# Optimization experiments

Hardware: AMD Instinct MI355X
Metric: run time of the kernel (lower is better)

The kernel has to match this reference:

```python
import jax, jax.numpy as jnp
import numpy as np

ML, KS, L = 3, 7, 7  # mL, kernelSize, L = 2*mL+1


def _conv(img, kern, pad, groups=1):
    # img: [N,C,H,W], kern: [O, C//groups, kh, kw]
    return jax.lax.conv_general_dilated(
        img, kern, (1, 1), [(pad, pad), (pad, pad)],
        dimension_numbers=("NCHW", "OIHW", "NCHW"),
        feature_group_count=groups)


def setup_inputs() -> dict:
    key = jax.random.key(0)
    ks = jax.random.split(key, 16)
    B, MU = 64, 256
    lin = lambda k, fi, fo: (jax.random.normal(k, (fi, fo), jnp.float32) / np.sqrt(fi)).astype(jnp.float32)
    return {
        "x": jax.random.normal(ks[0], (B, 1, MU, MU), jnp.float32),
        "f": jax.random.normal(ks[1], (B, 1, MU, MU), jnp.float32),
        "kernelA": jax.random.normal(ks[2], (B, 1, 3, 3), jnp.float32),
        "fc1_w1": lin(ks[3], 9, 200), "fc1_b1": jnp.zeros((200,), jnp.float32),
        "fc1_w2": lin(ks[4], 200, ML * KS * KS), "fc1_b2": jnp.zeros((ML * KS * KS,), jnp.float32),
        "fc2_w1": lin(ks[5], 9, 200), "fc2_b1": jnp.zeros((200,), jnp.float32),
        "fc2_w2": lin(ks[6], 200, ML * ML * KS * KS), "fc2_b2": jnp.zeros((ML * ML * KS * KS,), jnp.float32),
    }


def reference(x, f, kernelA, fc1_w1, fc1_b1, fc1_w2, fc1_b2, fc2_w1, fc2_b1, fc2_w2, fc2_b2):
    B, _, mu, _ = x.shape
    pad = KS // 2

    # residual r = f - A x   (per-sample 3x3 stencil conv, grouped)
    r = f - jax.vmap(lambda xi, ki: _conv(xi[None], ki[None], 1)[0])(x, kernelA)  # [B,1,mu,mu]

    # meta-MLPs produce per-sample dynamic conv kernels from the 3x3 stencil
    kA = kernelA.reshape(B, 9)
    h1 = jax.nn.relu(kA @ fc1_w1 + fc1_b1)
    w1 = (h1 @ fc1_w2 + fc1_b2).reshape(B, ML, 1, KS, KS)
    h2 = jax.nn.relu(kA @ fc2_w1 + fc2_b1)
    w2 = (h2 @ fc2_w2 + fc2_b2).reshape(B, ML, ML, KS, KS)

    # per-sample dynamic convs (batched via vmap)
    G1 = jax.vmap(lambda ri, wi: _conv(ri[None], wi, pad)[0])(r, w1)    # [B,mL,mu,mu]
    G2 = jax.vmap(lambda gi, wi: _conv(gi[None], wi, pad)[0])(G1, w2)   # [B,mL,mu,mu]
    G = jnp.concatenate([r, G1, G2], axis=1)                            # [B,L,mu,mu]

    # S = A G : apply per-sample stencil to each of the L channels (depthwise)
    S = jax.vmap(lambda gi, ki: _conv(gi[None], jnp.broadcast_to(ki[None], (L, 1, 3, 3)), 1, groups=L)[0])(G, kernelA)
    S = S.reshape(B, L, mu * mu)
    Gf = G.reshape(B, L, mu * mu)
    lr = r.reshape(B, mu * mu, 1)

    # normal equations: (S S^T) K = S r, tiny [L,L] solve per sample
    M = jnp.einsum("bln,bmn->blm", S, S)    # [B,L,L]
    b = jnp.matmul(S, lr)                   # [B,L,1]
    K = jnp.linalg.solve(M, b)              # [B,L,1]

    x_new = x + jnp.matmul(K.transpose(0, 2, 1), Gf).reshape(B, 1, mu, mu)
    return x_new
```

## Files before the change

kernel.cpp:

```cpp
#include <hip/hip_runtime.h>

#define MU 256
#define NPIX (MU*MU)
#define ML 3
#define KS 7
#define LCH 7
#define NENT 35
#define RBLK 64

__global__ void mlp_kernel(const float* __restrict__ kernelA,
                           const float* __restrict__ fc1_w1, const float* __restrict__ fc1_b1,
                           const float* __restrict__ fc1_w2, const float* __restrict__ fc1_b2,
                           const float* __restrict__ fc2_w1, const float* __restrict__ fc2_b1,
                           const float* __restrict__ fc2_w2, const float* __restrict__ fc2_b2,
                           float* __restrict__ w1_out, float* __restrict__ w2_out) {
    int b = blockIdx.x;
    int t = threadIdx.x;
    __shared__ float kA[9];
    __shared__ float h1[200], h2[200];
    if (t < 9) kA[t] = kernelA[b*9 + t];
    __syncthreads();
    if (t < 200) {
        float s1 = fc1_b1[t], s2 = fc2_b1[t];
        #pragma unroll
        for (int i = 0; i < 9; ++i) {
            s1 += kA[i] * fc1_w1[i*200 + t];
            s2 += kA[i] * fc2_w1[i*200 + t];
        }
        h1[t] = fmaxf(s1, 0.f);
        h2[t] = fmaxf(s2, 0.f);
    }
    __syncthreads();
    if (t < 147) {
        float s = fc1_b2[t];
        for (int i = 0; i < 200; ++i) s += h1[i] * fc1_w2[i*147 + t];
        w1_out[b*147 + t] = s;
    }
    for (int o = t; o < 441; o += 256) {
        float s = fc2_b2[o];
        for (int i = 0; i < 200; ++i) s += h2[i] * fc2_w2[i*441 + o];
        w2_out[b*441 + o] = s;
    }
}

__global__ __launch_bounds__(256, 4) void residual_kernel(
        const float* __restrict__ x, const float* __restrict__ f,
        const float* __restrict__ kA, float* __restrict__ r) {
    int b = blockIdx.z;
    __shared__ float tile[18][72];
    int tx = threadIdx.x, ty = threadIdx.y;
    int tid = ty*64 + tx;
    float k[9];
    #pragma unroll
    for (int i = 0; i < 9; ++i) k[i] = kA[b*9 + i];
    int x0 = blockIdx.x*64, ysub = blockIdx.y*16;
    const float* xb = x + (size_t)b*NPIX;

    for (int u = tid; u < 18*18; u += 256) {
        int row = u / 18, q4 = u % 18;
        int yy = ysub + row - 1;
        int xx = x0 - 4 + q4*4;
        float4 vv = make_float4(0.f, 0.f, 0.f, 0.f);
        if (yy >= 0 && yy < MU && xx >= 0 && xx < MU)
            vv = *(const float4*)(xb + yy*MU + xx);
        *(float4*)&tile[row][q4*4] = vv;
    }
    __syncthreads();

    int ry = ty*4;
    float S0 = 0.f, S1 = 0.f, S2 = 0.f, S3 = 0.f;
    #pragma unroll
    for (int t = 0; t < 6; ++t) {
        float v0 = tile[ry + t][tx + 3];
        float v1 = tile[ry + t][tx + 4];
        float v2 = tile[ry + t][tx + 5];
        float e0 = v0*k[0] + v1*k[1] + v2*k[2];
        float e1 = v0*k[3] + v1*k[4] + v2*k[5];
        float e2 = v0*k[6] + v1*k[7] + v2*k[8];
        if (t == 0) { S0 += e0; }
        if (t == 1) { S1 += e0; S0 += e1; }
        if (t == 2) { S2 += e0; S1 += e1; S0 += e2; }
        if (t == 3) { S3 += e0; S2 += e1; S1 += e2; }
        if (t == 4) {           S3 += e1; S2 += e2; }
        if (t == 5) {                     S3 += e2; }
    }
    float Sv[4] = {S0, S1, S2, S3};
    #pragma unroll
    for (int dy = 0; dy < 4; ++dy) {
        size_t p = (size_t)b*NPIX + (size_t)(ysub + ry + dy)*MU + x0 + tx;
        r[p] = f[p] - Sv[dy];
    }
}

__global__ __launch_bounds__(256) void conv7_g1(
        const float* __restrict__ r, const float* __restrict__ w1,
        float* __restrict__ G1) {
    int b = blockIdx.z;
    __shared__ float tile[22][136];
    int tx = threadIdx.x;
    int ty = threadIdx.y;
    int tid = ty*64 + tx;
    int x0 = blockIdx.x*128, y0 = blockIdx.y*16;
    const float* rb = r + (size_t)b*NPIX;
    const float* wgt = w1 + (size_t)b*147;

    for (int u = tid; u < 22*34; u += 256) {
        int row = u / 34, q4 = u % 34;
        int yy = y0 + row - 3;
        int xx = x0 - 4 + q4*4;
        float4 vv = make_float4(0.f, 0.f, 0.f, 0.f);
        if (yy >= 0 && yy < MU && xx >= 0 && xx < MU)
            vv = *(const float4*)(rb + yy*MU + xx);
        *(float4*)&tile[row][q4*4] = vv;
    }
    __syncthreads();

    float accA[3][4], accB[3][4];
    #pragma unroll
    for (int co = 0; co < 3; ++co)
        #pragma unroll
        for (int dy = 0; dy < 4; ++dy) { accA[co][dy] = 0.f; accB[co][dy] = 0.f; }

    int ry = ty*4;
    #pragma unroll
    for (int ir = 0; ir < 10; ++ir) {
        float v[10];
        #pragma unroll
        for (int h = 0; h < 5; ++h)
            *(float2*)&v[h*2] = *(float2*)&tile[ry + ir][2*tx + h*2];
        #pragma unroll
        for (int dy = 0; dy < 4; ++dy) {
            int i = ir - dy;
            if (i >= 0 && i <= 6) {
                #pragma unroll
                for (int co = 0; co < 3; ++co)
                    #pragma unroll
                    for (int j = 0; j < 7; ++j) {
                        float w = wgt[(co*7 + i)*7 + j];
                        accA[co][dy] += v[1 + j] * w;
                        accB[co][dy] += v[2 + j] * w;
                    }
            }
        }
    }
    #pragma unroll
    for (int dy = 0; dy < 4; ++dy) {
        size_t p = (size_t)b*3*NPIX + (size_t)(y0 + ry + dy)*MU + x0 + 2*tx;
        #pragma unroll
        for (int co = 0; co < 3; ++co)
            *(float2*)&G1[p + (size_t)co*NPIX] = make_float2(accA[co][dy], accB[co][dy]);
    }
}

__global__ __launch_bounds__(256) void conv7_g2(
        const float* __restrict__ G1, const float* __restrict__ w2,
        float* __restrict__ G2) {
    int b = blockIdx.z;
    __shared__ float tile[3][10][136];
    int tx = threadIdx.x;
    int ty = threadIdx.y;
    int tid = ty*64 + tx;
    int x0 = blockIdx.x*128, y0 = blockIdx.y*4;
    const float* g1b = G1 + (size_t)b*3*NPIX;
    const float* wgt = w2 + (size_t)b*441;

    for (int u = tid; u < 3*10*34; u += 256) {
        int c = u / (10*34);
        int rem = u % (10*34);
        int row = rem / 34, q4 = rem % 34;
        int yy = y0 + row - 3;
        int xx = x0 - 4 + q4*4;
        float4 vv = make_float4(0.f, 0.f, 0.f, 0.f);
        if (yy >= 0 && yy < MU && xx >= 0 && xx < MU)
            vv = *(const float4*)(g1b + (size_t)c*NPIX + yy*MU + xx);
        *(float4*)&tile[c][row][q4*4] = vv;
    }
    __syncthreads();

    float accA[3], accB[3];
    #pragma unroll
    for (int co = 0; co < 3; ++co) { accA[co] = 0.f; accB[co] = 0.f; }

    #pragma unroll
    for (int c = 0; c < 3; ++c) {
        #pragma unroll
        for (int ir = 0; ir < 7; ++ir) {
            float v[10];
            #pragma unroll
            for (int h = 0; h < 5; ++h)
                *(float2*)&v[h*2] = *(float2*)&tile[c][ty + ir][2*tx + h*2];
            #pragma unroll
            for (int co = 0; co < 3; ++co)
                #pragma unroll
                for (int j = 0; j < 7; ++j) {
                    float w = wgt[((co*3 + c)*7 + ir)*7 + j];
                    accA[co] += v[1 + j] * w;
                    accB[co] += v[2 + j] * w;
                }
        }
    }
    size_t p = (size_t)b*3*NPIX + (size_t)(y0 + ty)*MU + x0 + 2*tx;
    #pragma unroll
    for (int co = 0; co < 3; ++co)
        *(float2*)&G2[p + (size_t)co*NPIX] = make_float2(accA[co], accB[co]);
}

__global__ __launch_bounds__(256, 4) void reduce_kernel(
        const float* __restrict__ r, const float* __restrict__ G1,
        const float* __restrict__ G2, const float* __restrict__ kA,
        float* __restrict__ partial) {
    int b = blockIdx.z;
    __shared__ float tile[7][18][72];
    __shared__ float wsum[NENT][4];
    int tx = threadIdx.x;
    int ty = threadIdx.y;
    int tid = ty*64 + tx;
    float k[9];
    #pragma unroll
    for (int i = 0; i < 9; ++i) k[i] = kA[b*9 + i];

    const float* srcs[7] = {
        r  + (size_t)b*NPIX,
        G1 + (size_t)b*3*NPIX, G1 + (size_t)b*3*NPIX + NPIX, G1 + (size_t)b*3*NPIX + 2*NPIX,
        G2 + (size_t)b*3*NPIX, G2 + (size_t)b*3*NPIX + NPIX, G2 + (size_t)b*3*NPIX + 2*NPIX
    };

    int x0 = blockIdx.x*64;
    int ysub = blockIdx.y*16;

    #pragma unroll
    for (int c = 0; c < 7; ++c) {
        const float* src = srcs[c];
        for (int u = tid; u < 18*18; u += 256) {
            int row = u / 18, q4 = u % 18;
            int yy = ysub + row - 1;
            int xx = x0 - 4 + q4*4;
            float4 vv = make_float4(0.f, 0.f, 0.f, 0.f);
            if (yy >= 0 && yy < MU && xx >= 0 && xx < MU)
                vv = *(const float4*)(src + yy*MU + xx);
            *(float4*)&tile[c][row][q4*4] = vv;
        }
    }
    __syncthreads();

    float acc[64];
    #pragma unroll
    for (int e = 0; e < 64; ++e) acc[e] = 0.f;

    int ry = ty*4;
    float S_all[7][4];
    #pragma unroll
    for (int c = 0; c < 7; ++c) {
        float S0 = 0.f, S1 = 0.f, S2 = 0.f, S3 = 0.f;
        #pragma unroll
        for (int t = 0; t < 6; ++t) {
            float v0 = tile[c][ry + t][tx + 3];
            float v1 = tile[c][ry + t][tx + 4];
            float v2 = tile[c][ry + t][tx + 5];
            float e0 = v0*k[0] + v1*k[1] + v2*k[2];
            float e1 = v0*k[3] + v1*k[4] + v2*k[5];
            float e2 = v0*k[6] + v1*k[7] + v2*k[8];
            if (t == 0) { S0 += e0; }
            if (t == 1) { S1 += e0; S0 += e1; }
            if (t == 2) { S2 += e0; S1 += e1; S0 += e2; }
            if (t == 3) { S3 += e0; S2 += e1; S1 += e2; }
            if (t == 4) {           S3 += e1; S2 += e2; }
            if (t == 5) {                     S3 += e2; }
        }
        S_all[c][0] = S0; S_all[c][1] = S1; S_all[c][2] = S2; S_all[c][3] = S3;
    }
    #pragma unroll
    for (int dy = 0; dy < 4; ++dy) {
        float rv = tile[0][ry + dy + 1][tx + 4];
        int idx = 0;
        #pragma unroll
        for (int l = 0; l < 7; ++l) {
            #pragma unroll
            for (int m = l; m < 7; ++m) {
                acc[idx] += S_all[l][dy] * S_all[m][dy];
                ++idx;
            }
        }
        #pragma unroll
        for (int l = 0; l < 7; ++l) acc[28 + l] += S_all[l][dy] * rv;
    }

    #pragma unroll
    for (int step = 0; step < 6; ++step) {
        const int mask = 1 << step;
        const int nh = 32 >> step;
        bool hi = (tx & mask) != 0;
        #pragma unroll
        for (int i = 0; i < nh; ++i) {
            float send = hi ? acc[i] : acc[i + nh];
            float got = __shfl_xor(send, mask);
            acc[i] = (hi ? acc[i + nh] : acc[i]) + got;
        }
    }
    int ent = ((tx&1)<<5) | ((tx&2)<<3) | ((tx&4)<<1)
            | ((tx&8)>>1) | ((tx&16)>>3) | ((tx&32)>>5);
    if (ent < NENT) wsum[ent][ty] = acc[0];
    __syncthreads();
    if (tid < NENT) {
        float s = wsum[tid][0] + wsum[tid][1] + wsum[tid][2] + wsum[tid][3];
        int blockLinear = blockIdx.y*4 + blockIdx.x;
        partial[((size_t)b*NENT + tid)*RBLK + blockLinear] = s;
    }
}

__global__ void reduce2_kernel(const float* __restrict__ partial,
                               double* __restrict__ M, double* __restrict__ bv) {
    int b = blockIdx.x;
    int wave = threadIdx.x >> 6;
    int lane = threadIdx.x & 63;
    for (int e = wave; e < NENT; e += 4) {
        const float* p = partial + ((size_t)b*NENT + e)*RBLK;
        double s = (double)p[lane];
        #pragma unroll
        for (int off = 32; off; off >>= 1) s += __shfl_down(s, off);
        if (lane == 0) {
            if (e < 28) M[b*28 + e] = s;
            else        bv[b*7 + (e - 28)] = s;
        }
    }
}

__global__ __launch_bounds__(64, 1) void solve_kernel(
        const double* __restrict__ M, const double* __restrict__ bv,
        float* __restrict__ K, int B) {
    int b = blockIdx.x*64 + threadIdx.x;
    if (b >= B) return;
    double A[7][8];
    int idx = 0;
    #pragma unroll
    for (int l = 0; l < 7; ++l)
        #pragma unroll
        for (int m = l; m < 7; ++m) {
            double v = M[b*28 + idx];
            A[l][m] = v;
            A[m][l] = v;
            ++idx;
        }
    #pragma unroll
    for (int l = 0; l < 7; ++l) A[l][7] = bv[b*7 + l];

    #pragma unroll
    for (int col = 0; col < 7; ++col) {
        int piv = col;
        double mx = fabs(A[col][col]);
        #pragma unroll
        for (int rr = 0; rr < 7; ++rr) {
            if (rr > col) {
                double a = fabs(A[rr][col]);
                if (a > mx) { mx = a; piv = rr; }
            }
        }
        #pragma unroll
        for (int rr = 0; rr < 7; ++rr) {
            if (rr > col) {
                bool c = (rr == piv);
                #pragma unroll
                for (int cc = 0; cc < 8; ++cc) {
                    double t0 = A[col][cc], t1 = A[rr][cc];
                    A[col][cc] = c ? t1 : t0;
                    A[rr][cc]  = c ? t0 : t1;
                }
            }
        }
        double d = A[col][col];
        #pragma unroll
        for (int rr = 0; rr < 7; ++rr) {
            if (rr > col) {
                double fct = A[rr][col] / d;
                #pragma unroll
                for (int cc = 0; cc < 8; ++cc) A[rr][cc] -= fct * A[col][cc];
            }
        }
    }
    double Kv[7];
    #pragma unroll
    for (int rr = 6; rr >= 0; --rr) {
        double s = A[rr][7];
        #pragma unroll
        for (int cc = 0; cc < 7; ++cc)
            if (cc > rr) s -= A[rr][cc] * Kv[cc];
        Kv[rr] = s / A[rr][rr];
    }
    #pragma unroll
    for (int l = 0; l < 7; ++l) K[b*7 + l] = (float)Kv[l];
}

__global__ void update_kernel(const float* __restrict__ x, const float* __restrict__ r,
                              const float* __restrict__ G1, const float* __restrict__ G2,
                              const float* __restrict__ K, float* __restrict__ out) {
    int b = blockIdx.z;
    int p4 = blockIdx.x*256 + threadIdx.x;
    float k0 = K[b*7+0], k1 = K[b*7+1], k2 = K[b*7+2], k3 = K[b*7+3];
    float k4 = K[b*7+4], k5 = K[b*7+5], k6 = K[b*7+6];
    size_t q  = (size_t)b*(NPIX/4) + p4;
    size_t q3 = (size_t)b*3*(NPIX/4) + p4;
    const float4* x4  = (const float4*)x;
    const float4* r4  = (const float4*)r;
    const float4* g14 = (const float4*)G1;
    const float4* g24 = (const float4*)G2;
    float4 xv = x4[q], rv = r4[q];
    float4 a = g14[q3], bb = g14[q3 + NPIX/4], c = g14[q3 + 2*(NPIX/4)];
    float4 d = g24[q3], e  = g24[q3 + NPIX/4], g = g24[q3 + 2*(NPIX/4)];
    float4 o;
    o.x = xv.x + k0*rv.x + k1*a.x + k2*bb.x + k3*c.x + k4*d.x + k5*e.x + k6*g.x;
    o.y = xv.y + k0*rv.y + k1*a.y + k2*bb.y + k3*c.y + k4*d.y + k5*e.y + k6*g.y;
    o.z = xv.z + k0*rv.z + k1*a.z + k2*bb.z + k3*c.z + k4*d.z + k5*e.z + k6*g.z;
    o.w = xv.w + k0*rv.w + k1*a.w + k2*bb.w + k3*c.w + k4*d.w + k5*e.w + k6*g.w;
    ((float4*)out)[q] = o;
}

extern "C" void kernel_launch(void* const* d_in, const int* in_sizes, int n_in,
                              void* d_out, int out_size, void* d_ws, size_t ws_size,
                              hipStream_t stream) {
    const float* x       = (const float*)d_in[0];
    const float* f       = (const float*)d_in[1];
    const float* kernelA = (const float*)d_in[2];
    const float* fc1_w1  = (const float*)d_in[3];
    const float* fc1_b1  = (const float*)d_in[4];
    const float* fc1_w2  = (const float*)d_in[5];
    const float* fc1_b2  = (const float*)d_in[6];
    const float* fc2_w1  = (const float*)d_in[7];
    const float* fc2_b1  = (const float*)d_in[8];
    const float* fc2_w2  = (const float*)d_in[9];
    const float* fc2_b2  = (const float*)d_in[10];
    float* out = (float*)d_out;

    const int B = in_sizes[2] / 9;

    double* Mws = (double*)d_ws;
    double* bws = Mws + (size_t)B*28;
    float*  w1  = (float*)(bws + (size_t)B*7);
    float*  w2  = w1 + (size_t)B*147;
    float*  Kv  = w2 + (size_t)B*441;
    float*  r   = Kv + (size_t)B*7 + 1;
    float*  G1  = r  + (size_t)B*NPIX;
    float*  G2  = G1 + (size_t)B*3*NPIX;
    float*  partial = G2 + (size_t)B*3*NPIX;

    dim3 cblk(64, 4);
    dim3 rgrd(MU/64, MU/16, B);
    dim3 g1grd(MU/128, MU/16, B);
    dim3 g2grd(MU/128, MU/4, B);

    hipLaunchKernelGGL(mlp_kernel, dim3(B), dim3(256), 0, stream,
                       kernelA, fc1_w1, fc1_b1, fc1_w2, fc1_b2,
                       fc2_w1, fc2_b1, fc2_w2, fc2_b2, w1, w2);
    hipLaunchKernelGGL(residual_kernel, rgrd, cblk, 0, stream, x, f, kernelA, r);
    hipLaunchKernelGGL(conv7_g1, g1grd, cblk, 0, stream, r, w1, G1);
    hipLaunchKernelGGL(conv7_g2, g2grd, cblk, 0, stream, G1, w2, G2);
    hipLaunchKernelGGL(reduce_kernel, rgrd, cblk, 0, stream, r, G1, G2, kernelA, partial);
    hipLaunchKernelGGL(reduce2_kernel, dim3(B), dim3(256), 0, stream, partial, Mws, bws);
    hipLaunchKernelGGL(solve_kernel, dim3((B + 63)/64), dim3(64), 0, stream, Mws, bws, Kv, B);
    hipLaunchKernelGGL(update_kernel, dim3(NPIX/1024, 1, B), dim3(256), 0, stream,
                       x, r, G1, G2, Kv, out);
}
```

Baseline: 206.9 us.

## Fuse G2 convolution into Gram reduction kernel with haloed recompute

Merges the 7x7 G2 convolution and the S/Gram-matrix reduction into one kernel. Each 64x16 block loads a larger G1 halo, computes G2 (including a 1-pixel halo) into shared memory, writes the interior to global, and then builds S and the partial normal-equation sums from shared tiles. This removes one launch and the global re-read of G2 and G1 in the reduction. In exchange the halo G2 values are recomputed redundantly, the block uses more shared memory and registers, and it loses the __launch_bounds__ occupancy hint of 4.

```diff
diff --git a/kernel.cpp b/kernel.cpp
--- a/kernel.cpp
+++ b/kernel.cpp
@@ -152,111 +152,89 @@
     }
 }
 
-__global__ __launch_bounds__(256) void conv7_g2(
-        const float* __restrict__ G1, const float* __restrict__ w2,
-        float* __restrict__ G2) {
+__global__ __launch_bounds__(256) void g2gram_kernel(
+        const float* __restrict__ G1, const float* __restrict__ r,
+        const float* __restrict__ w2, const float* __restrict__ kA,
+        float* __restrict__ G2, float* __restrict__ partial) {
     int b = blockIdx.z;
-    __shared__ float tile[3][10][136];
-    int tx = threadIdx.x;
-    int ty = threadIdx.y;
-    int tid = ty*64 + tx;
-    int x0 = blockIdx.x*128, y0 = blockIdx.y*4;
-    const float* g1b = G1 + (size_t)b*3*NPIX;
-    const float* wgt = w2 + (size_t)b*441;
-
-    for (int u = tid; u < 3*10*34; u += 256) {
-        int c = u / (10*34);
-        int rem = u % (10*34);
-        int row = rem / 34, q4 = rem % 34;
-        int yy = y0 + row - 3;
-        int xx = x0 - 4 + q4*4;
-        float4 vv = make_float4(0.f, 0.f, 0.f, 0.f);
-        if (yy >= 0 && yy < MU && xx >= 0 && xx < MU)
-            vv = *(const float4*)(g1b + (size_t)c*NPIX + yy*MU + xx);
-        *(float4*)&tile[c][row][q4*4] = vv;
-    }
-    __syncthreads();
-
-    float accA[3], accB[3];
-    #pragma unroll
-    for (int co = 0; co < 3; ++co) { accA[co] = 0.f; accB[co] = 0.f; }
-
-    #pragma unroll
-    for (int c = 0; c < 3; ++c) {
-        #pragma unroll
-        for (int ir = 0; ir < 7; ++ir) {
-            float v[10];
-            #pragma unroll
-            for (int h = 0; h < 5; ++h)
-                *(float2*)&v[h*2] = *(float2*)&tile[c][ty + ir][2*tx + h*2];
-            #pragma unroll
-            for (int co = 0; co < 3; ++co)
-                #pragma unroll
-                for (int j = 0; j < 7; ++j) {
-                    float w = wgt[((co*3 + c)*7 + ir)*7 + j];
-                    accA[co] += v[1 + j] * w;
-                    accB[co] += v[2 + j] * w;
-                }
-        }
-    }
-    size_t p = (size_t)b*3*NPIX + (size_t)(y0 + ty)*MU + x0 + 2*tx;
-    #pragma unroll
-    for (int co = 0; co < 3; ++co)
-        *(float2*)&G2[p + (size_t)co*NPIX] = make_float2(accA[co], accB[co]);
-}
-
-__global__ __launch_bounds__(256, 4) void reduce_kernel(
-        const float* __restrict__ r, const float* __restrict__ G1,
-        const float* __restrict__ G2, const float* __restrict__ kA,
-        float* __restrict__ partial) {
-    int b = blockIdx.z;
-    __shared__ float tile[7][18][72];
+    __shared__ float g1t[3][24][80];
+    __shared__ float g2t[3][18][68];
+    __shared__ float rt[18][72];
     __shared__ float wsum[NENT][4];
     int tx = threadIdx.x;
     int ty = threadIdx.y;
     int tid = ty*64 + tx;
+    int x0 = blockIdx.x*64, y0 = blockIdx.y*16;
+    const float* g1b = G1 + (size_t)b*3*NPIX;
+    const float* rb  = r  + (size_t)b*NPIX;
+    const float* wgt = w2 + (size_t)b*441;
     float k[9];
     #pragma unroll
     for (int i = 0; i < 9; ++i) k[i] = kA[b*9 + i];
 
-    const float* srcs[7] = {
-        r  + (size_t)b*NPIX,
-        G1 + (size_t)b*3*NPIX, G1 + (size_t)b*3*NPIX + NPIX, G1 + (size_t)b*3*NPIX + 2*NPIX,
-        G2 + (size_t)b*3*NPIX, G2 + (size_t)b*3*NPIX + NPIX, G2 + (size_t)b*3*NPIX + 2*NPIX
-    };
-
-    int x0 = blockIdx.x*64;
-    int ysub = blockIdx.y*16;
-
-    #pragma unroll
-    for (int c = 0; c < 7; ++c) {
-        const float* src = srcs[c];
-        for (int u = tid; u < 18*18; u += 256) {
-            int row = u / 18, q4 = u % 18;
-            int yy = ysub + row - 1;
-            int xx = x0 - 4 + q4*4;
-            float4 vv = make_float4(0.f, 0.f, 0.f, 0.f);
-            if (yy >= 0 && yy < MU && xx >= 0 && xx < MU)
-                vv = *(const float4*)(src + yy*MU + xx);
-            *(float4*)&tile[c][row][q4*4] = vv;
-        }
-    }
-    __syncthreads();
-
-    float acc[64];
-    #pragma unroll
-    for (int e = 0; e < 64; ++e) acc[e] = 0.f;
+    for (int u = tid; u < 3*24*20; u += 256) {
+        int c = u / (24*20);
+        int rem = u % (24*20);
+        int row = rem / 20, q4 = rem % 20;
+        int yy = y0 + row - 4;
+        int xx = x0 - 8 + q4*4;
+        float4 vv = make_float4(0.f, 0.f, 0.f, 0.f);
+        if (yy >= 0 && yy < MU && xx >= 0 && xx < MU)
+            vv = *(const float4*)(g1b + (size_t)c*NPIX + yy*MU + xx);
+        *(float4*)&g1t[c][row][q4*4] = vv;
+    }
+    for (int u = tid; u < 18*18; u += 256) {
+        int row = u / 18, q4 = u % 18;
+        int yy = y0 + row - 1;
+        int xx = x0 - 4 + q4*4;
+        float4 vv = make_float4(0.f, 0.f, 0.f, 0.f);
+        if (yy >= 0 && yy < MU && xx >= 0 && xx < MU)
+            vv = *(const float4*)(rb + yy*MU + xx);
+        *(float4*)&rt[row][q4*4] = vv;
+    }
+    __syncthreads();
+
+    for (int t = tid; t < 18*34; t += 256) {
+        int row = t / 34, p = t % 34;
+        float accA[3] = {0.f, 0.f, 0.f}, accB[3] = {0.f, 0.f, 0.f};
+        #pragma unroll
+        for (int c = 0; c < 3; ++c)
+            #pragma unroll
+            for (int ir = 0; ir < 7; ++ir) {
+                float v[10];
+                #pragma unroll
+                for (int h = 0; h < 5; ++h)
+                    *(float2*)&v[2*h] = *(float2*)&g1t[c][row + ir][2*p + 2 + 2*h];
+                #pragma unroll
+                for (int co = 0; co < 3; ++co)
+                    #pragma unroll
+                    for (int j = 0; j < 7; ++j) {
+                        float w = wgt[((co*3 + c)*7 + ir)*7 + j];
+                        accA[co] += v[1 + j] * w;
+                        accB[co] += v[2 + j] * w;
+                    }
+            }
+        #pragma unroll
+        for (int co = 0; co < 3; ++co)
+            *(float2*)&g2t[co][row][2*p] = make_float2(accA[co], accB[co]);
+        if (row >= 1 && row <= 16 && p >= 1 && p <= 32) {
+            size_t q = (size_t)b*3*NPIX + (size_t)(y0 + row - 1)*MU + (x0 - 2 + 2*p);
+            #pragma unroll
+            for (int co = 0; co < 3; ++co)
+                *(float2*)&G2[q + (size_t)co*NPIX] = make_float2(accA[co], accB[co]);
+        }
+    }
+    __syncthreads();
 
     int ry = ty*4;
     float S_all[7][4];
-    #pragma unroll
-    for (int c = 0; c < 7; ++c) {
+    {
         float S0 = 0.f, S1 = 0.f, S2 = 0.f, S3 = 0.f;
         #pragma unroll
         for (int t = 0; t < 6; ++t) {
-            float v0 = tile[c][ry + t][tx + 3];
-            float v1 = tile[c][ry + t][tx + 4];
-            float v2 = tile[c][ry + t][tx + 5];
+            float v0 = rt[ry + t][tx + 3];
+            float v1 = rt[ry + t][tx + 4];
+            float v2 = rt[ry + t][tx + 5];
             float e0 = v0*k[0] + v1*k[1] + v2*k[2];
             float e1 = v0*k[3] + v1*k[4] + v2*k[5];
             float e2 = v0*k[6] + v1*k[7] + v2*k[8];
@@ -267,11 +245,58 @@
             if (t == 4) {           S3 += e1; S2 += e2; }
             if (t == 5) {                     S3 += e2; }
         }
-        S_all[c][0] = S0; S_all[c][1] = S1; S_all[c][2] = S2; S_all[c][3] = S3;
-    }
+        S_all[0][0] = S0; S_all[0][1] = S1; S_all[0][2] = S2; S_all[0][3] = S3;
+    }
+    #pragma unroll
+    for (int ci = 0; ci < 3; ++ci) {
+        float S0 = 0.f, S1 = 0.f, S2 = 0.f, S3 = 0.f;
+        #pragma unroll
+        for (int t = 0; t < 6; ++t) {
+            float v0 = g1t[ci][ry + 3 + t][tx + 7];
+            float v1 = g1t[ci][ry + 3 + t][tx + 8];
+            float v2 = g1t[ci][ry + 3 + t][tx + 9];
+            float e0 = v0*k[0] + v1*k[1] + v2*k[2];
+            float e1 = v0*k[3] + v1*k[4] + v2*k[5];
+            float e2 = v0*k[6] + v1*k[7] + v2*k[8];
+            if (t == 0) { S0 += e0; }
+            if (t == 1) { S1 += e0; S0 += e1; }
+            if (t == 2) { S2 += e0; S1 += e1; S0 += e2; }
+            if (t == 3) { S3 += e0; S2 += e1; S1 += e2; }
+            if (t == 4) {           S3 += e1; S2 += e2; }
+            if (t == 5) {                     S3 += e2; }
+        }
+        S_all[1 + ci][0] = S0; S_all[1 + ci][1] = S1;
+        S_all[1 + ci][2] = S2; S_all[1 + ci][3] = S3;
+    }
+    #pragma unroll
+    for (int ci = 0; ci < 3; ++ci) {
+        float S0 = 0.f, S1 = 0.f, S2 = 0.f, S3 = 0.f;
+        #pragma unroll
+        for (int t = 0; t < 6; ++t) {
+            float v0 = g2t[ci][ry + t][tx + 1];
+            float v1 = g2t[ci][ry + t][tx + 2];
+            float v2 = g2t[ci][ry + t][tx + 3];
+            float e0 = v0*k[0] + v1*k[1] + v2*k[2];
+            float e1 = v0*k[3] + v1*k[4] + v2*k[5];
+            float e2 = v0*k[6] + v1*k[7] + v2*k[8];
+            if (t == 0) { S0 += e0; }
+            if (t == 1) { S1 += e0; S0 += e1; }
+            if (t == 2) { S2 += e0; S1 += e1; S0 += e2; }
+            if (t == 3) { S3 += e0; S2 += e1; S1 += e2; }
+            if (t == 4) {           S3 += e1; S2 += e2; }
+            if (t == 5) {                     S3 += e2; }
+        }
+        S_all[4 + ci][0] = S0; S_all[4 + ci][1] = S1;
+        S_all[4 + ci][2] = S2; S_all[4 + ci][3] = S3;
+    }
+
+    float acc[64];
+    #pragma unroll
+    for (int e = 0; e < 64; ++e) acc[e] = 0.f;
+
     #pragma unroll
     for (int dy = 0; dy < 4; ++dy) {
-        float rv = tile[0][ry + dy + 1][tx + 4];
+        float rv = rt[ry + dy + 1][tx + 4];
         int idx = 0;
         #pragma unroll
         for (int l = 0; l < 7; ++l) {
@@ -445,15 +470,13 @@
     dim3 cblk(64, 4);
     dim3 rgrd(MU/64, MU/16, B);
     dim3 g1grd(MU/128, MU/16, B);
-    dim3 g2grd(MU/128, MU/4, B);
 
     hipLaunchKernelGGL(mlp_kernel, dim3(B), dim3(256), 0, stream,
                        kernelA, fc1_w1, fc1_b1, fc1_w2, fc1_b2,
                        fc2_w1, fc2_b1, fc2_w2, fc2_b2, w1, w2);
     hipLaunchKernelGGL(residual_kernel, rgrd, cblk, 0, stream, x, f, kernelA, r);
     hipLaunchKernelGGL(conv7_g1, g1grd, cblk, 0, stream, r, w1, G1);
-    hipLaunchKernelGGL(conv7_g2, g2grd, cblk, 0, stream, G1, w2, G2);
-    hipLaunchKernelGGL(reduce_kernel, rgrd, cblk, 0, stream, r, G1, G2, kernelA, partial);
+    hipLaunchKernelGGL(g2gram_kernel, rgrd, cblk, 0, stream, G1, r, w2, kernelA, G2, partial);
     hipLaunchKernelGGL(reduce2_kernel, dim3(B), dim3(256), 0, stream, partial, Mws, bws);
     hipLaunchKernelGGL(solve_kernel, dim3((B + 63)/64), dim3(64), 0, stream, Mws, bws, Kv, B);
     hipLaunchKernelGGL(update_kernel, dim3(NPIX/1024, 1, B), dim3(256), 0, stream,
```

After: 272.4 us. 1.32x slower.
